# Performance work log

Measured on AMD Instinct MI355X. Metric: run time of the kernel, lower is better.

## Reference

```python
import math
import jax, jax.numpy as jnp
import numpy as np

DIM = 1536; NH = 12; HD = DIM // NH        # head_dim = 128
F, H, W = 4, 20, 26
S = F * H * W                              # 2080 tokens
BLOCK = 128
SPAD = math.ceil(S / BLOCK) * BLOCK        # 2176
EPS = 1e-6
C = HD // 2
SF, SH, SW = C - 2 * (C // 3), C // 3, C // 3   # 22, 21, 21 rotary bands


def _rope_params(max_len, d, theta=10000.0):
    inv = 1.0 / (theta ** (np.arange(0, d, 2, dtype=np.float64) / d))
    return np.outer(np.arange(max_len), inv)   # [max_len, d//2] angles


def _rope(x, freqs, f, h, w):
    # x: [b, s, n, d] with s == f*h*w; freqs: [1024, d//2] angles
    b, s, n, d = x.shape
    ang = jnp.concatenate([
        jnp.broadcast_to(freqs[:f, :SF][:, None, None, :], (f, h, w, SF)),
        jnp.broadcast_to(freqs[:h, SF:SF + SH][None, :, None, :], (f, h, w, SH)),
        jnp.broadcast_to(freqs[:w, SF + SH:C][None, None, :, :], (f, h, w, SW)),
    ], axis=-1).reshape(s, C)
    cos = jnp.cos(ang)[None, :, None, :]
    sin = jnp.sin(ang)[None, :, None, :]
    xr = x.reshape(b, s, n, C, 2)
    x0, x1 = xr[..., 0], xr[..., 1]          # complex mult (x0+ix1)*(cos+isin)
    out = jnp.stack([x0 * cos - x1 * sin, x0 * sin + x1 * cos], axis=-1)
    return out.reshape(b, s, n, d)


def setup_inputs():
    key = jax.random.key(0)
    ks = jax.random.split(key, 6)
    freqs = jnp.asarray(np.concatenate([
        _rope_params(1024, 2 * SF), _rope_params(1024, 2 * SH), _rope_params(1024, 2 * SW)
    ], axis=1), dtype=jnp.float32)           # [1024, 64]
    lin = lambda k: jax.random.normal(k, (DIM, DIM), jnp.float32) * 0.02
    blk = jnp.arange(SPAD) // BLOCK
    # block-causal (128-token blocks) mask, padding keys (>= S) masked out
    mask = (blk[:, None] >= blk[None, :]) & (jnp.arange(SPAD)[None, :] < S)
    return {
        "x": jax.random.normal(ks[0], (1, S, DIM), jnp.float32),
        "freqs": freqs,
        "wq": lin(ks[1]), "bq": jnp.zeros((DIM,), jnp.float32),
        "wk": lin(ks[2]), "bk": jnp.zeros((DIM,), jnp.float32),
        "wv": lin(ks[3]), "bv": jnp.zeros((DIM,), jnp.float32),
        "wo": lin(ks[4]), "bo": jnp.zeros((DIM,), jnp.float32),
        "gq": jnp.ones((DIM,), jnp.float32),
        "gk": jnp.ones((DIM,), jnp.float32),
        "seq_lens": jnp.array([S], jnp.int32),
        "grid_sizes": jnp.array([[F, H, W]], jnp.int32),
        "mask": mask,
    }


def reference(x, freqs, wq, bq, wk, bk, wv, bv, wo, bo, gq, gk, seq_lens, grid_sizes, mask):
    b, s, _ = x.shape
    n, d = NH, HD
    rms = lambda t, g: (t * jax.lax.rsqrt(jnp.mean(t * t, axis=-1, keepdims=True) + EPS)) * g
    q = rms(x @ wq + bq, gq).reshape(b, s, n, d)
    k = rms(x @ wk + bk, gk).reshape(b, s, n, d)
    v = (x @ wv + bv).reshape(b, s, n, d)
    f, h, w = int(grid_sizes[0, 0]), int(grid_sizes[0, 1]), int(grid_sizes[0, 2])
    sl = int(seq_lens[0])
    if sl > 0 and s == 2 * sl:  # teacher forcing: rope each half independently
        q = jnp.concatenate([_rope(q[:, :sl], freqs, f, h, w), _rope(q[:, sl:], freqs, f, h, w)], axis=1)
        k = jnp.concatenate([_rope(k[:, :sl], freqs, f, h, w), _rope(k[:, sl:], freqs, f, h, w)], axis=1)
    else:
        q = _rope(q, freqs, f, h, w)
        k = _rope(k, freqs, f, h, w)
    pad = SPAD - s
    if pad > 0:
        pz = ((0, 0), (0, pad), (0, 0), (0, 0))
        q, k, v = jnp.pad(q, pz), jnp.pad(k, pz), jnp.pad(v, pz)
    scores = jnp.einsum('bqnd,bknd->bnqk', q, k) / math.sqrt(d)
    scores = jnp.where(mask[None, None], scores, -jnp.inf)
    attn = jax.nn.softmax(scores, axis=-1)
    o = jnp.einsum('bnqk,bknd->bqnd', attn, v)[:, :s].reshape(b, s, n * d)
    return o @ wo + bo
```

## Files before the change

### kernel.cpp

```cpp
#include <hip/hip_runtime.h>

#define DIMM   1536
#define NHEAD  12
#define HD     128
#define SEQ    2080
#define SPADN  2176
#define HWPROD 520
#define SCALE  0.08838834764831845f
#define K2F    0.12751744154f

typedef short short8  __attribute__((ext_vector_type(8)));
typedef float floatx4 __attribute__((ext_vector_type(4)));

__device__ __forceinline__ unsigned short f2bf(float f) {
    union { float f; unsigned u; } v; v.f = f;
    return (unsigned short)((v.u + 0x7fffu + ((v.u >> 16) & 1u)) >> 16);
}
__device__ __forceinline__ float bf2f(unsigned short u) {
    union { unsigned u; float f; } v; v.u = ((unsigned)u) << 16;
    return v.f;
}

__device__ __forceinline__ void gld_lds16(const void* g, void* l) {
    __builtin_amdgcn_global_load_lds(
        (const __attribute__((address_space(1))) unsigned int*)g,
        (__attribute__((address_space(3))) unsigned int*)l, 16, 0, 0);
}

__constant__ int c_base[33] = {0,1,2,3,4,5,6,7,
                               8,10,12,14,16,18,20,22,
                               24,27,30,33,36,39,42,45,
                               48,52,56,60,64,68,72,76,
                               80};
#define SLOTS_PER_HEAD 85

__global__ void k_prep(const float* __restrict__ x,
                       const float* __restrict__ w0, const float* __restrict__ w1,
                       const float* __restrict__ w2, const float* __restrict__ w3,
                       unsigned short* __restrict__ xb,
                       unsigned short* __restrict__ t0, unsigned short* __restrict__ t1,
                       unsigned short* __restrict__ t2, unsigned short* __restrict__ t3) {
    int z = blockIdx.z;
    if (z == 4) {
        int n4 = SEQ * DIMM / 4;
        int idx = (blockIdx.y * 24 + blockIdx.x) * 256 + threadIdx.x;
#pragma unroll
        for (int i = 0; i < 6; i++) {
            int p = idx + i * 147456;
            if (p < n4) {
                float4 v = ((const float4*)x)[p];
                ushort4 o;
                o.x = f2bf(v.x); o.y = f2bf(v.y); o.z = f2bf(v.z); o.w = f2bf(v.w);
                ((ushort4*)xb)[p] = o;
            }
        }
        return;
    }
    const float* in = (z == 0) ? w0 : (z == 1) ? w1 : (z == 2) ? w2 : w3;
    unsigned short* out = (z == 0) ? t0 : (z == 1) ? t1 : (z == 2) ? t2 : t3;
    __shared__ float tile[64][65];
    int tx = threadIdx.x & 63, ty = threadIdx.x >> 6;
    int r0 = blockIdx.x * 64, c0 = blockIdx.y * 64;
#pragma unroll
    for (int i = 0; i < 16; i++)
        tile[i * 4 + ty][tx] = in[(size_t)(r0 + i * 4 + ty) * DIMM + c0 + tx];
    __syncthreads();
#pragma unroll
    for (int i = 0; i < 16; i++) {
        int cc = i * 4 + ty;
        out[(size_t)(c0 + cc) * DIMM + r0 + tx] = f2bf(tile[tx][cc]);
    }
}

__global__ __launch_bounds__(256, 3) void k_gemm(
    const unsigned short* __restrict__ A,
    const unsigned short* __restrict__ B0, const unsigned short* __restrict__ B1,
    const unsigned short* __restrict__ B2,
    const float* __restrict__ bias0, const float* __restrict__ bias1, const float* __restrict__ bias2,
    unsigned short* __restrict__ Qh, unsigned short* __restrict__ Kh,
    unsigned short* __restrict__ Vt,
    int M, int N, int K) {
    const unsigned short* B = B0; const float* bias = bias0;
    if (blockIdx.z == 1) { B = B1; bias = bias1; }
    if (blockIdx.z == 2) { B = B2; bias = bias2; }

    __shared__ unsigned short As[128 * 64];
    __shared__ unsigned short Bs[128 * 64];

    int tid = threadIdx.x;
    int lane = tid & 63, wv = tid >> 6;
    int quad = lane >> 4, l16 = lane & 15;
    int m0 = blockIdx.y * 128, n0 = blockIdx.x * 128;
    int wm = (wv >> 1) * 64, wn = (wv & 1) * 64;
    int sw = l16 & 7;

    int srow_in_blk = lane >> 3;
    int schunk = lane & 7;
    int gchunk = schunk ^ (srow_in_blk & 7);

    floatx4 acc[4][4];
#pragma unroll
    for (int i = 0; i < 4; i++)
#pragma unroll
        for (int j = 0; j < 4; j++) acc[i][j] = (floatx4){0.f, 0.f, 0.f, 0.f};

    for (int k0 = 0; k0 < K; k0 += 64) {
#pragma unroll
        for (int i = 0; i < 4; i++) {
            int blkrow = (wv * 4 + i) * 8;
            int r = blkrow + srow_in_blk;
            int ra = m0 + r; if (ra > M - 1) ra = M - 1;
            gld_lds16(A + (size_t)ra * K + k0 + gchunk * 8, &As[blkrow * 64]);
            gld_lds16(B + (size_t)(n0 + r) * K + k0 + gchunk * 8, &Bs[blkrow * 64]);
        }
        __syncthreads();
#pragma unroll
        for (int kc = 0; kc < 2; kc++) {
            short8 af[4], bfr[4];
#pragma unroll
            for (int t = 0; t < 4; t++) {
                int ca = ((kc * 4 + quad) ^ sw) << 3;
                af[t]  = *(const short8*)&As[(wm + t * 16 + l16) * 64 + ca];
                bfr[t] = *(const short8*)&Bs[(wn + t * 16 + l16) * 64 + ca];
            }
#pragma unroll
            for (int mi = 0; mi < 4; mi++)
#pragma unroll
                for (int ni = 0; ni < 4; ni++)
                    acc[mi][ni] = __builtin_amdgcn_mfma_f32_16x16x32_bf16(af[mi], bfr[ni], acc[mi][ni], 0, 0, 0);
        }
        __syncthreads();
    }
    if (blockIdx.z == 2) {
#pragma unroll
        for (int mi = 0; mi < 4; mi++) {
            int row0 = m0 + wm + mi * 16 + quad * 4;
            if (row0 < M) {
#pragma unroll
                for (int ni = 0; ni < 4; ni++) {
                    int col = n0 + wn + ni * 16 + l16;
                    float b = bias[col];
                    ushort4 o;
                    o.x = f2bf(acc[mi][ni][0] + b);
                    o.y = f2bf(acc[mi][ni][1] + b);
                    o.z = f2bf(acc[mi][ni][2] + b);
                    o.w = f2bf(acc[mi][ni][3] + b);
                    *(ushort4*)(Vt + (size_t)col * SPADN + row0) = o;
                }
            }
        }
    } else {
        unsigned short* O = (blockIdx.z == 0) ? Qh : Kh;
#pragma unroll
        for (int mi = 0; mi < 4; mi++) {
#pragma unroll
            for (int r = 0; r < 4; r++) {
                int row = m0 + wm + mi * 16 + quad * 4 + r;
                if (row < M) {
#pragma unroll
                    for (int ni = 0; ni < 4; ni++) {
                        int col = n0 + wn + ni * 16 + l16;
                        O[(size_t)row * DIMM + col] = f2bf(acc[mi][ni][r] + bias[col]);
                    }
                }
            }
        }
    }
}

__global__ __launch_bounds__(256, 8) void k_gemm64(
    const unsigned short* __restrict__ A, const unsigned short* __restrict__ B,
    const float* __restrict__ bias, float* __restrict__ C, int M, int N, int K) {
    __shared__ unsigned short As[64 * 64];
    __shared__ unsigned short Bs[64 * 64];
    int tid = threadIdx.x;
    int lane = tid & 63, wv = tid >> 6;
    int quad = lane >> 4, l16 = lane & 15;
    int m0 = blockIdx.y * 64, n0 = blockIdx.x * 64;
    int wm = (wv >> 1) * 32, wn = (wv & 1) * 32;

    int srow = lane >> 3;
    int schunk = lane & 7;

    floatx4 acc[2][2];
#pragma unroll
    for (int i = 0; i < 2; i++)
#pragma unroll
        for (int j = 0; j < 2; j++) acc[i][j] = (floatx4){0.f, 0.f, 0.f, 0.f};

    for (int k0 = 0; k0 < K; k0 += 64) {
#pragma unroll
        for (int i = 0; i < 2; i++) {
            int rb = (i * 4 + wv) * 8;
            int r = rb + srow;
            int g = schunk ^ (r & 7);
            int ra = m0 + r; if (ra > M - 1) ra = M - 1;
            gld_lds16(A + (size_t)ra * K + k0 + g * 8, &As[rb * 64]);
            gld_lds16(B + (size_t)(n0 + r) * K + k0 + g * 8, &Bs[rb * 64]);
        }
        __syncthreads();
#pragma unroll
        for (int kc = 0; kc < 2; kc++) {
            short8 af[2], bfr[2];
#pragma unroll
            for (int t = 0; t < 2; t++) {
                int rowa = wm + t * 16 + l16;
                int rowb = wn + t * 16 + l16;
                int c = kc * 4 + quad;
                af[t]  = *(const short8*)&As[rowa * 64 + ((c ^ (rowa & 7)) << 3)];
                bfr[t] = *(const short8*)&Bs[rowb * 64 + ((c ^ (rowb & 7)) << 3)];
            }
#pragma unroll
            for (int mi = 0; mi < 2; mi++)
#pragma unroll
                for (int ni = 0; ni < 2; ni++)
                    acc[mi][ni] = __builtin_amdgcn_mfma_f32_16x16x32_bf16(af[mi], bfr[ni], acc[mi][ni], 0, 0, 0);
        }
        __syncthreads();
    }
#pragma unroll
    for (int mi = 0; mi < 2; mi++) {
#pragma unroll
        for (int r = 0; r < 4; r++) {
            int row = m0 + wm + mi * 16 + quad * 4 + r;
            if (row < M) {
#pragma unroll
                for (int ni = 0; ni < 2; ni++) {
                    int col = n0 + wn + ni * 16 + l16;
                    C[(size_t)row * N + col] = acc[mi][ni][r] + bias[col];
                }
            }
        }
    }
}

__global__ void k_rmsrope(const unsigned short* __restrict__ Qh, const unsigned short* __restrict__ Kh,
                          const float* __restrict__ gq, const float* __restrict__ gk,
                          const float* __restrict__ freqs,
                          unsigned short* __restrict__ Qa, unsigned short* __restrict__ Ka) {
    __shared__ float redq[4], redk[4];
    int s = blockIdx.x;
    int tid = threadIdx.x;
    int lane = tid & 63, wv = tid >> 6;
    const ushort2* qrow = (const ushort2*)(Qh + (size_t)s * DIMM);
    const ushort2* krow = (const ushort2*)(Kh + (size_t)s * DIMM);
    const float2* g2q = (const float2*)gq;
    const float2* g2k = (const float2*)gk;

    float2 qv[3], kv[3];
    float sq = 0.f, sk = 0.f;
#pragma unroll
    for (int j = 0; j < 3; j++) {
        int p = tid + j * 256;
        ushort2 uq = qrow[p], uk = krow[p];
        qv[j].x = bf2f(uq.x); qv[j].y = bf2f(uq.y);
        kv[j].x = bf2f(uk.x); kv[j].y = bf2f(uk.y);
        sq += qv[j].x * qv[j].x + qv[j].y * qv[j].y;
        sk += kv[j].x * kv[j].x + kv[j].y * kv[j].y;
    }
#pragma unroll
    for (int m = 32; m >= 1; m >>= 1) { sq += __shfl_xor(sq, m); sk += __shfl_xor(sk, m); }
    if (lane == 0) { redq[wv] = sq; redk[wv] = sk; }
    __syncthreads();
    float tq = redq[0] + redq[1] + redq[2] + redq[3];
    float tk = redk[0] + redk[1] + redk[2] + redk[3];
    float scq = rsqrtf(tq * (1.f / DIMM) + 1e-6f);
    float sck = rsqrtf(tk * (1.f / DIMM) + 1e-6f);

    int fi = s / HWPROD;
    int rem = s - fi * HWPROD;
    int hi = rem / 26;
    int wi = rem - hi * 26;
#pragma unroll
    for (int j = 0; j < 3; j++) {
        int p = tid + j * 256;
        int c = p & 63;
        int pos = (c < 22) ? fi : ((c < 43) ? hi : wi);
        float ang = freqs[pos * 64 + c];
        float sn, cs;
        __sincosf(ang, &sn, &cs);
        float2 gqa = g2q[p];
        float q0 = qv[j].x * scq * gqa.x, q1 = qv[j].y * scq * gqa.y;
        ushort2 oq; oq.x = f2bf(q0 * cs - q1 * sn); oq.y = f2bf(q0 * sn + q1 * cs);
        float2 gka = g2k[p];
        float kk0 = kv[j].x * sck * gka.x, kk1 = kv[j].y * sck * gka.y;
        ushort2 ok; ok.x = f2bf(kk0 * cs - kk1 * sn); ok.y = f2bf(kk0 * sn + kk1 * cs);
        int h = p >> 6;
        size_t off = ((size_t)h * SPADN + s) * HD + 2 * c;
        *(ushort2*)(Qa + off) = oq;
        *(ushort2*)(Ka + off) = ok;
    }
}

__global__ __launch_bounds__(256, 3) void k_attn1(const unsigned short* __restrict__ Qa,
                                                  const unsigned short* __restrict__ Ka,
                                                  const unsigned short* __restrict__ Vt,
                                                  float* __restrict__ Opart,
                                                  float* __restrict__ Lpart) {
    int j = blockIdx.x, h = blockIdx.y, z = blockIdx.z;
    int nkb = (j >> 1) * 2 + 2;
    if (nkb > 33) nkb = 33;
    int kb0 = z * 8;
    if (kb0 >= nkb) return;
    int kb1 = kb0 + 8; if (kb1 > nkb) kb1 = nkb;

    __shared__ unsigned short Ks[64 * 128];
    __shared__ unsigned short Vs[128 * 64];
    __shared__ unsigned short Ps[4][16][72];

    int tid = threadIdx.x;
    int lane = tid & 63, wv = tid >> 6;
    int quad = lane >> 4, l16 = lane & 15;
    int qrow0 = j * 64 + wv * 16;

    short8 qf[4];
#pragma unroll
    for (int kc = 0; kc < 4; kc++)
        qf[kc] = *(const short8*)(Qa + ((size_t)h * SPADN + qrow0 + l16) * HD + kc * 32 + quad * 8);

    short8 ones8;
#pragma unroll
    for (int i = 0; i < 8; i++) ones8[i] = (short)0x3F80;

    floatx4 of[8], of9;
#pragma unroll
    for (int ni = 0; ni < 8; ni++) of[ni] = (floatx4){0.f, 0.f, 0.f, 0.f};
    of9 = (floatx4){0.f, 0.f, 0.f, 0.f};

    int krow = lane >> 4;
    int kslot = lane & 15;
    int vrow = lane >> 3;
    int vslot = lane & 7;

    for (int kb = kb0; kb < kb1; kb++) {
        const unsigned short* kbase = Ka + (((size_t)h * SPADN + kb * 64) * HD);
#pragma unroll
        for (int i = 0; i < 4; i++) {
            int rb = i * 4 + wv;
            int r = rb * 4 + krow;
            int g = (kslot & 8) | ((kslot & 7) ^ (r & 7));
            gld_lds16(kbase + r * 128 + g * 8, &Ks[rb * 512]);
        }
#pragma unroll
        for (int i = 0; i < 4; i++) {
            int rb = i * 4 + wv;
            int r = rb * 8 + vrow;
            int g = vslot ^ (r & 7);
            gld_lds16(Vt + ((size_t)h * HD + r) * SPADN + kb * 64 + g * 8, &Vs[rb * 512]);
        }
        __syncthreads();

        floatx4 sa[4];
#pragma unroll
        for (int ni = 0; ni < 4; ni++) sa[ni] = (floatx4){0.f, 0.f, 0.f, 0.f};
#pragma unroll
        for (int kc = 0; kc < 4; kc++) {
            int c = kc * 4 + quad;
            short8 kf[4];
#pragma unroll
            for (int ni = 0; ni < 4; ni++) {
                int row = ni * 16 + l16;
                int slot = (c & 8) | ((c & 7) ^ (row & 7));
                kf[ni] = *(const short8*)&Ks[row * 128 + slot * 8];
            }
#pragma unroll
            for (int ni = 0; ni < 4; ni++)
                sa[ni] = __builtin_amdgcn_mfma_f32_16x16x32_bf16(qf[kc], kf[ni], sa[ni], 0, 0, 0);
        }

        bool maskb = (kb == 32);
#pragma unroll
        for (int r = 0; r < 4; r++) {
#pragma unroll
            for (int ni = 0; ni < 4; ni++) {
                float xv = sa[ni][r] * K2F;
                if (maskb && (kb * 64 + ni * 16 + l16 >= SEQ)) xv = -1e30f;
                float p = exp2f(fminf(xv, 36.f));
                Ps[wv][quad * 4 + r][ni * 16 + l16] = f2bf(p);
            }
        }
#pragma unroll
        for (int kc = 0; kc < 2; kc++) {
            int ko = kc * 32 + quad * 8;
            short8 pf = *(const short8*)&Ps[wv][l16][ko];
            int c = kc * 4 + quad;
#pragma unroll
            for (int ni = 0; ni < 8; ni++) {
                int row = ni * 16 + l16;
                short8 vf = *(const short8*)&Vs[row * 64 + ((c ^ (row & 7)) << 3)];
                of[ni] = __builtin_amdgcn_mfma_f32_16x16x32_bf16(pf, vf, of[ni], 0, 0, 0);
            }
            of9 = __builtin_amdgcn_mfma_f32_16x16x32_bf16(pf, ones8, of9, 0, 0, 0);
        }
        __syncthreads();
    }

    int slot = h * SLOTS_PER_HEAD + c_base[j] + z;
    float* Op = Opart + (size_t)slot * 8192;
#pragma unroll
    for (int r = 0; r < 4; r++) {
        int lrow = wv * 16 + quad * 4 + r;
#pragma unroll
        for (int ni = 0; ni < 8; ni++)
            Op[lrow * 128 + ni * 16 + l16] = of[ni][r];
    }
    if (l16 == 0) {
#pragma unroll
        for (int r = 0; r < 4; r++)
            Lpart[slot * 64 + wv * 16 + quad * 4 + r] = of9[r];
    }
}

__global__ void k_attn2(const float* __restrict__ Opart,
                        const float* __restrict__ Lpart,
                        unsigned short* __restrict__ Ob) {
    int j = blockIdx.x, h = blockIdx.y;
    int nkb = (j >> 1) * 2 + 2; if (nkb > 33) nkb = 33;
    int nc = (nkb + 7) >> 3;
    int base = h * SLOTS_PER_HEAD + c_base[j];
    int t = threadIdx.x;
    int r = t >> 2;
    int c0 = (t & 3) * 32;
    int row = j * 64 + r;
    if (row >= SEQ) return;

    float acc[32];
#pragma unroll
    for (int q = 0; q < 32; q++) acc[q] = 0.f;
    float L = 0.f;
    for (int c = 0; c < nc; c++) {
        L += Lpart[(base + c) * 64 + r];
        const float4* op = (const float4*)(Opart + (size_t)(base + c) * 8192 + r * 128 + c0);
#pragma unroll
        for (int q = 0; q < 8; q++) {
            float4 v = op[q];
            acc[q * 4 + 0] += v.x; acc[q * 4 + 1] += v.y;
            acc[q * 4 + 2] += v.z; acc[q * 4 + 3] += v.w;
        }
    }
    float inv = 1.f / L;
    unsigned short* ob = Ob + (size_t)row * DIMM + h * HD + c0;
#pragma unroll
    for (int q = 0; q < 8; q++) {
        ushort4 o;
        o.x = f2bf(acc[q * 4 + 0] * inv); o.y = f2bf(acc[q * 4 + 1] * inv);
        o.z = f2bf(acc[q * 4 + 2] * inv); o.w = f2bf(acc[q * 4 + 3] * inv);
        *(ushort4*)(ob + q * 4) = o;
    }
}

extern "C" void kernel_launch(void* const* d_in, const int* in_sizes, int n_in,
                              void* d_out, int out_size, void* d_ws, size_t ws_size,
                              hipStream_t stream) {
    const float* x     = (const float*)d_in[0];
    const float* freqs = (const float*)d_in[1];
    const float* wq    = (const float*)d_in[2];
    const float* bq    = (const float*)d_in[3];
    const float* wk    = (const float*)d_in[4];
    const float* bk    = (const float*)d_in[5];
    const float* wv    = (const float*)d_in[6];
    const float* bv    = (const float*)d_in[7];
    const float* wo    = (const float*)d_in[8];
    const float* bo    = (const float*)d_in[9];
    const float* gq    = (const float*)d_in[10];
    const float* gk    = (const float*)d_in[11];
    float* out = (float*)d_out;

    char* ws = (char*)d_ws;
    size_t off = 0;
    auto alloc = [&](size_t bytes) -> void* {
        void* p = ws + off;
        off += (bytes + 255) & ~(size_t)255;
        return p;
    };
    unsigned short* xb  = (unsigned short*)alloc((size_t)SPADN * DIMM * 2);
    unsigned short* wqT = (unsigned short*)alloc((size_t)DIMM * DIMM * 2);
    unsigned short* wkT = (unsigned short*)alloc((size_t)DIMM * DIMM * 2);
    unsigned short* wvT = (unsigned short*)alloc((size_t)DIMM * DIMM * 2);
    unsigned short* Qh  = (unsigned short*)alloc((size_t)SEQ * DIMM * 2);
    unsigned short* Kh  = (unsigned short*)alloc((size_t)SEQ * DIMM * 2);
    unsigned short* woT = (unsigned short*)alloc((size_t)DIMM * DIMM * 2);
    unsigned short* Qa  = (unsigned short*)alloc((size_t)NHEAD * SPADN * HD * 2);
    unsigned short* Ka  = (unsigned short*)alloc((size_t)NHEAD * SPADN * HD * 2);
    unsigned short* Vt  = (unsigned short*)alloc((size_t)DIMM * SPADN * 2);
    unsigned short* Ob  = (unsigned short*)alloc((size_t)SEQ * DIMM * 2);
    float* Lpart = (float*)alloc((size_t)12 * SLOTS_PER_HEAD * 64 * 4);
    float* Opart = (float*)ws;
    (void)ws_size; (void)in_sizes; (void)n_in; (void)out_size;

    k_prep<<<dim3(24, 24, 5), 256, 0, stream>>>(x, wq, wk, wv, wo, xb, wqT, wkT, wvT, woT);
    k_gemm<<<dim3(12, 17, 3), 256, 0, stream>>>(xb, wqT, wkT, wvT, bq, bk, bv,
                                                Qh, Kh, Vt, SEQ, DIMM, DIMM);
    k_rmsrope<<<SEQ, 256, 0, stream>>>(Qh, Kh, gq, gk, freqs, Qa, Ka);
    k_attn1<<<dim3(33, 12, 5), 256, 0, stream>>>(Qa, Ka, Vt, Opart, Lpart);
    k_attn2<<<dim3(33, 12), 256, 0, stream>>>(Opart, Lpart, Ob);
    k_gemm64<<<dim3(24, 33), 256, 0, stream>>>(Ob, woT, bo, out, SEQ, DIMM, DIMM);
}
```

Before: 238.0 us.

## Use 128-row query tiles in attention with bf16 partials and direct single-chunk output

Each attention block now covers 128 query rows (32 per wave, two MFMA row tiles), so every K/V tile staged in LDS is reused across twice as many queries and the grid halves. Split-K partial outputs are stored as bf16 instead of fp32 to cut partial-sum traffic. Blocks that need only one key chunk write the normalized result straight to Ob, and the reduction kernel skips those rows. The cost is higher register pressure from doubled accumulators, possible loss of occupancy, and bf16 rounding of partials before the final reduction.

```diff
diff --git a/kernel.cpp b/kernel.cpp
--- a/kernel.cpp
+++ b/kernel.cpp
@@ -27,12 +27,8 @@
         (__attribute__((address_space(3))) unsigned int*)l, 16, 0, 0);
 }
 
-__constant__ int c_base[33] = {0,1,2,3,4,5,6,7,
-                               8,10,12,14,16,18,20,22,
-                               24,27,30,33,36,39,42,45,
-                               48,52,56,60,64,68,72,76,
-                               80};
-#define SLOTS_PER_HEAD 85
+__constant__ int c_base2[17] = {0,1,2,3,4,6,8,10,12,15,18,21,24,28,32,36,40};
+#define SLOTS2_PER_HEAD 45
 
 __global__ void k_prep(const float* __restrict__ x,
                        const float* __restrict__ w0, const float* __restrict__ w1,
@@ -295,37 +291,44 @@
 __global__ __launch_bounds__(256, 3) void k_attn1(const unsigned short* __restrict__ Qa,
                                                   const unsigned short* __restrict__ Ka,
                                                   const unsigned short* __restrict__ Vt,
-                                                  float* __restrict__ Opart,
-                                                  float* __restrict__ Lpart) {
+                                                  unsigned short* __restrict__ Opart,
+                                                  float* __restrict__ Lpart,
+                                                  unsigned short* __restrict__ Ob) {
     int j = blockIdx.x, h = blockIdx.y, z = blockIdx.z;
-    int nkb = (j >> 1) * 2 + 2;
+    int nkb = 2 * j + 2;
     if (nkb > 33) nkb = 33;
+    int nc = (nkb + 7) >> 3;
+    if (z >= nc) return;
     int kb0 = z * 8;
-    if (kb0 >= nkb) return;
     int kb1 = kb0 + 8; if (kb1 > nkb) kb1 = nkb;
 
     __shared__ unsigned short Ks[64 * 128];
     __shared__ unsigned short Vs[128 * 64];
-    __shared__ unsigned short Ps[4][16][72];
+    __shared__ unsigned short Ps[4][32][72];
 
     int tid = threadIdx.x;
     int lane = tid & 63, wv = tid >> 6;
     int quad = lane >> 4, l16 = lane & 15;
-    int qrow0 = j * 64 + wv * 16;
-
-    short8 qf[4];
-#pragma unroll
-    for (int kc = 0; kc < 4; kc++)
-        qf[kc] = *(const short8*)(Qa + ((size_t)h * SPADN + qrow0 + l16) * HD + kc * 32 + quad * 8);
+    int qrow0 = j * 128 + wv * 32;
+
+    short8 qf[2][4];
+#pragma unroll
+    for (int mi = 0; mi < 2; mi++)
+#pragma unroll
+        for (int kc = 0; kc < 4; kc++)
+            qf[mi][kc] = *(const short8*)(Qa + ((size_t)h * SPADN + qrow0 + mi * 16 + l16) * HD + kc * 32 + quad * 8);
 
     short8 ones8;
 #pragma unroll
     for (int i = 0; i < 8; i++) ones8[i] = (short)0x3F80;
 
-    floatx4 of[8], of9;
-#pragma unroll
-    for (int ni = 0; ni < 8; ni++) of[ni] = (floatx4){0.f, 0.f, 0.f, 0.f};
-    of9 = (floatx4){0.f, 0.f, 0.f, 0.f};
+    floatx4 of[2][8], of9[2];
+#pragma unroll
+    for (int mi = 0; mi < 2; mi++) {
+#pragma unroll
+        for (int ni = 0; ni < 8; ni++) of[mi][ni] = (floatx4){0.f, 0.f, 0.f, 0.f};
+        of9[mi] = (floatx4){0.f, 0.f, 0.f, 0.f};
+    }
 
     int krow = lane >> 4;
     int kslot = lane & 15;
@@ -350,9 +353,11 @@
         }
         __syncthreads();
 
-        floatx4 sa[4];
-#pragma unroll
-        for (int ni = 0; ni < 4; ni++) sa[ni] = (floatx4){0.f, 0.f, 0.f, 0.f};
+        floatx4 sa[2][4];
+#pragma unroll
+        for (int mi = 0; mi < 2; mi++)
+#pragma unroll
+            for (int ni = 0; ni < 4; ni++) sa[mi][ni] = (floatx4){0.f, 0.f, 0.f, 0.f};
 #pragma unroll
         for (int kc = 0; kc < 4; kc++) {
             int c = kc * 4 + quad;
@@ -364,84 +369,116 @@
                 kf[ni] = *(const short8*)&Ks[row * 128 + slot * 8];
             }
 #pragma unroll
-            for (int ni = 0; ni < 4; ni++)
-                sa[ni] = __builtin_amdgcn_mfma_f32_16x16x32_bf16(qf[kc], kf[ni], sa[ni], 0, 0, 0);
+            for (int mi = 0; mi < 2; mi++)
+#pragma unroll
+                for (int ni = 0; ni < 4; ni++)
+                    sa[mi][ni] = __builtin_amdgcn_mfma_f32_16x16x32_bf16(qf[mi][kc], kf[ni], sa[mi][ni], 0, 0, 0);
         }
 
         bool maskb = (kb == 32);
 #pragma unroll
-        for (int r = 0; r < 4; r++) {
-#pragma unroll
-            for (int ni = 0; ni < 4; ni++) {
-                float xv = sa[ni][r] * K2F;
-                if (maskb && (kb * 64 + ni * 16 + l16 >= SEQ)) xv = -1e30f;
-                float p = exp2f(fminf(xv, 36.f));
-                Ps[wv][quad * 4 + r][ni * 16 + l16] = f2bf(p);
+        for (int mi = 0; mi < 2; mi++) {
+#pragma unroll
+            for (int r = 0; r < 4; r++) {
+#pragma unroll
+                for (int ni = 0; ni < 4; ni++) {
+                    float xv = sa[mi][ni][r] * K2F;
+                    if (maskb && (kb * 64 + ni * 16 + l16 >= SEQ)) xv = -1e30f;
+                    float p = exp2f(fminf(xv, 36.f));
+                    Ps[wv][mi * 16 + quad * 4 + r][ni * 16 + l16] = f2bf(p);
+                }
             }
         }
 #pragma unroll
         for (int kc = 0; kc < 2; kc++) {
             int ko = kc * 32 + quad * 8;
-            short8 pf = *(const short8*)&Ps[wv][l16][ko];
             int c = kc * 4 + quad;
+            short8 pf[2];
+#pragma unroll
+            for (int mi = 0; mi < 2; mi++) pf[mi] = *(const short8*)&Ps[wv][mi * 16 + l16][ko];
 #pragma unroll
             for (int ni = 0; ni < 8; ni++) {
                 int row = ni * 16 + l16;
                 short8 vf = *(const short8*)&Vs[row * 64 + ((c ^ (row & 7)) << 3)];
-                of[ni] = __builtin_amdgcn_mfma_f32_16x16x32_bf16(pf, vf, of[ni], 0, 0, 0);
-            }
-            of9 = __builtin_amdgcn_mfma_f32_16x16x32_bf16(pf, ones8, of9, 0, 0, 0);
+#pragma unroll
+                for (int mi = 0; mi < 2; mi++)
+                    of[mi][ni] = __builtin_amdgcn_mfma_f32_16x16x32_bf16(pf[mi], vf, of[mi][ni], 0, 0, 0);
+            }
+#pragma unroll
+            for (int mi = 0; mi < 2; mi++)
+                of9[mi] = __builtin_amdgcn_mfma_f32_16x16x32_bf16(pf[mi], ones8, of9[mi], 0, 0, 0);
         }
         __syncthreads();
     }
 
-    int slot = h * SLOTS_PER_HEAD + c_base[j] + z;
-    float* Op = Opart + (size_t)slot * 8192;
-#pragma unroll
-    for (int r = 0; r < 4; r++) {
-        int lrow = wv * 16 + quad * 4 + r;
-#pragma unroll
-        for (int ni = 0; ni < 8; ni++)
-            Op[lrow * 128 + ni * 16 + l16] = of[ni][r];
-    }
-    if (l16 == 0) {
-#pragma unroll
-        for (int r = 0; r < 4; r++)
-            Lpart[slot * 64 + wv * 16 + quad * 4 + r] = of9[r];
-    }
-}
-
-__global__ void k_attn2(const float* __restrict__ Opart,
+    if (nc == 1) {
+#pragma unroll
+        for (int mi = 0; mi < 2; mi++) {
+#pragma unroll
+            for (int r = 0; r < 4; r++) {
+                float inv = 1.f / of9[mi][r];
+                int row = qrow0 + mi * 16 + quad * 4 + r;
+#pragma unroll
+                for (int ni = 0; ni < 8; ni++)
+                    Ob[(size_t)row * DIMM + h * HD + ni * 16 + l16] = f2bf(of[mi][ni][r] * inv);
+            }
+        }
+    } else {
+        int slot = h * SLOTS2_PER_HEAD + c_base2[j] + z;
+        unsigned short* Op = Opart + (size_t)slot * 16384;
+#pragma unroll
+        for (int mi = 0; mi < 2; mi++) {
+#pragma unroll
+            for (int r = 0; r < 4; r++) {
+                int lrow = wv * 32 + mi * 16 + quad * 4 + r;
+#pragma unroll
+                for (int ni = 0; ni < 8; ni++)
+                    Op[lrow * 128 + ni * 16 + l16] = f2bf(of[mi][ni][r]);
+            }
+        }
+        if (l16 == 0) {
+#pragma unroll
+            for (int mi = 0; mi < 2; mi++)
+#pragma unroll
+                for (int r = 0; r < 4; r++)
+                    Lpart[slot * 128 + wv * 32 + mi * 16 + quad * 4 + r] = of9[mi][r];
+        }
+    }
+}
+
+__global__ void k_attn2(const unsigned short* __restrict__ Opart,
                         const float* __restrict__ Lpart,
                         unsigned short* __restrict__ Ob) {
     int j = blockIdx.x, h = blockIdx.y;
-    int nkb = (j >> 1) * 2 + 2; if (nkb > 33) nkb = 33;
+    int nkb = 2 * j + 2; if (nkb > 33) nkb = 33;
     int nc = (nkb + 7) >> 3;
-    int base = h * SLOTS_PER_HEAD + c_base[j];
+    if (nc == 1) return;
+    int base = h * SLOTS2_PER_HEAD + c_base2[j];
     int t = threadIdx.x;
-    int r = t >> 2;
-    int c0 = (t & 3) * 32;
-    int row = j * 64 + r;
-    if (row >= SEQ) return;
-
-    float acc[32];
-#pragma unroll
-    for (int q = 0; q < 32; q++) acc[q] = 0.f;
+    int row = t >> 1;
+    int dh = (t & 1) * 64;
+    int grow = j * 128 + row;
+    if (grow >= SEQ) return;
+
+    float acc[64];
+#pragma unroll
+    for (int q = 0; q < 64; q++) acc[q] = 0.f;
     float L = 0.f;
     for (int c = 0; c < nc; c++) {
-        L += Lpart[(base + c) * 64 + r];
-        const float4* op = (const float4*)(Opart + (size_t)(base + c) * 8192 + r * 128 + c0);
-#pragma unroll
-        for (int q = 0; q < 8; q++) {
-            float4 v = op[q];
-            acc[q * 4 + 0] += v.x; acc[q * 4 + 1] += v.y;
-            acc[q * 4 + 2] += v.z; acc[q * 4 + 3] += v.w;
+        int slot = base + c;
+        L += Lpart[slot * 128 + row];
+        const ushort4* op = (const ushort4*)(Opart + (size_t)slot * 16384 + row * 128 + dh);
+#pragma unroll
+        for (int q = 0; q < 16; q++) {
+            ushort4 u = op[q];
+            acc[q * 4 + 0] += bf2f(u.x); acc[q * 4 + 1] += bf2f(u.y);
+            acc[q * 4 + 2] += bf2f(u.z); acc[q * 4 + 3] += bf2f(u.w);
         }
     }
     float inv = 1.f / L;
-    unsigned short* ob = Ob + (size_t)row * DIMM + h * HD + c0;
-#pragma unroll
-    for (int q = 0; q < 8; q++) {
+    unsigned short* ob = Ob + (size_t)grow * DIMM + h * HD + dh;
+#pragma unroll
+    for (int q = 0; q < 16; q++) {
         ushort4 o;
         o.x = f2bf(acc[q * 4 + 0] * inv); o.y = f2bf(acc[q * 4 + 1] * inv);
         o.z = f2bf(acc[q * 4 + 2] * inv); o.w = f2bf(acc[q * 4 + 3] * inv);
@@ -484,15 +521,15 @@
     unsigned short* Ka  = (unsigned short*)alloc((size_t)NHEAD * SPADN * HD * 2);
     unsigned short* Vt  = (unsigned short*)alloc((size_t)DIMM * SPADN * 2);
     unsigned short* Ob  = (unsigned short*)alloc((size_t)SEQ * DIMM * 2);
-    float* Lpart = (float*)alloc((size_t)12 * SLOTS_PER_HEAD * 64 * 4);
-    float* Opart = (float*)ws;
+    float* Lpart = (float*)alloc((size_t)12 * SLOTS2_PER_HEAD * 128 * 4);
+    unsigned short* Opart = (unsigned short*)ws;
     (void)ws_size; (void)in_sizes; (void)n_in; (void)out_size;
 
     k_prep<<<dim3(24, 24, 5), 256, 0, stream>>>(x, wq, wk, wv, wo, xb, wqT, wkT, wvT, woT);
     k_gemm<<<dim3(12, 17, 3), 256, 0, stream>>>(xb, wqT, wkT, wvT, bq, bk, bv,
                                                 Qh, Kh, Vt, SEQ, DIMM, DIMM);
     k_rmsrope<<<SEQ, 256, 0, stream>>>(Qh, Kh, gq, gk, freqs, Qa, Ka);
-    k_attn1<<<dim3(33, 12, 5), 256, 0, stream>>>(Qa, Ka, Vt, Opart, Lpart);
-    k_attn2<<<dim3(33, 12), 256, 0, stream>>>(Opart, Lpart, Ob);
+    k_attn1<<<dim3(17, 12, 5), 256, 0, stream>>>(Qa, Ka, Vt, Opart, Lpart, Ob);
+    k_attn2<<<dim3(17, 12), 256, 0, stream>>>(Opart, Lpart, Ob);
     k_gemm64<<<dim3(24, 33), 256, 0, stream>>>(Ob, woT, bo, out, SEQ, DIMM, DIMM);
 }
```

New measurement: 271.4 us. 14.0% more time.
